# Kernel optimization log

Measured on AMD Instinct MI355X. Metric: run time of the kernel, lower is better.

## Reference

```python
import jax, jax.numpy as jnp
import numpy as np

USER_COUNT = 100000
ITEM_COUNT = 50000
N_NODES = USER_COUNT + ITEM_COUNT
NNZ = 4800000
EMB = 64
BATCH = 4096


def setup_inputs() -> dict:
    key = jax.random.key(0)
    k1, k2, k3, k4, k5, k6, k7 = jax.random.split(key, 7)
    return {
        "user_emb": jax.random.normal(k1, (USER_COUNT, EMB), dtype=jnp.float32),
        "item_emb": jax.random.normal(k2, (ITEM_COUNT, EMB), dtype=jnp.float32),
        "adj_vals": jax.random.uniform(k3, (NNZ,), dtype=jnp.float32),
        "adj_row": jax.random.randint(k4, (NNZ,), 0, N_NODES, dtype=jnp.int64),
        "adj_col": jax.random.randint(k5, (NNZ,), 0, N_NODES, dtype=jnp.int64),
        "users": jax.random.randint(k6, (BATCH,), 0, USER_COUNT, dtype=jnp.int64),
        "items": jax.random.randint(k7, (BATCH,), 0, ITEM_COUNT, dtype=jnp.int64),
        "n_layers": 3,
    }


def _spmm(adj_row, adj_col, adj_vals, x):
    # sparse (N,N) @ dense (N,D): gather source rows, scale by edge values, scatter-add to dest
    msgs = adj_vals[:, None] * x[adj_col]  # [nnz, D]
    return jax.ops.segment_sum(msgs, adj_row, num_segments=N_NODES)


def reference(user_emb, item_emb, adj_vals, adj_row, adj_col, users, items, n_layers):
    ego = jnp.concatenate([user_emb, item_emb], axis=0)  # [N, D]
    for _ in range(n_layers):
        ego = _spmm(adj_row, adj_col, adj_vals, ego)
    user_all = ego[:USER_COUNT]
    item_all = ego[USER_COUNT:]
    return (user_all[users], item_all[items])
```

## Files before the change

### kernel.cpp

```cpp
#include <hip/hip_runtime.h>
#include <hip/hip_bf16.h>

#define USER_COUNT 100000
#define ITEM_COUNT 50000
#define N_NODES    150000
#define EMB        64
#define BATCH      4096

#define NFINE      586
#define FSHIFT     8
#define STRIDE     8960
#define TILE_E     6400

__device__ inline unsigned short f2bf_raw(float f) {
    __hip_bfloat16 h = __float2bfloat16(f);
    unsigned short u; __builtin_memcpy(&u, &h, 2); return u;
}

__global__ __launch_bounds__(256) void zero_kernel(int* __restrict__ p, int n) {
    int i = blockIdx.x * blockDim.x + threadIdx.x;
    if (i < n) p[i] = 0;
}

__global__ __launch_bounds__(512) void partition_kernel(
        const float* __restrict__ vals,
        const int* __restrict__ rows,
        const int* __restrict__ cols,
        int* __restrict__ gcur,
        uint2* __restrict__ fine, int nnz) {
    __shared__ uint2 buf[TILE_E];
    __shared__ unsigned short bid[TILE_E];
    __shared__ int   cnt[NFINE];
    __shared__ int   sloff[NFINE + 1];
    __shared__ int   gb[NFINE];
    __shared__ int   sscan[512];
    const int b = blockIdx.x, t = threadIdx.x;
    const int sbeg = b * TILE_E, send = min(sbeg + TILE_E, nnz);
    const int n = send - sbeg;

    for (int f = t; f < NFINE; f += 512) cnt[f] = 0;
    __syncthreads();
    for (int i = sbeg + t; i < send; i += 512)
        atomicAdd(&cnt[rows[i] >> FSHIFT], 1);
    __syncthreads();
    int c0 = (2 * t < NFINE) ? cnt[2 * t] : 0;
    int c1 = (2 * t + 1 < NFINE) ? cnt[2 * t + 1] : 0;
    sscan[t] = c0 + c1;
    __syncthreads();
    for (int o = 1; o < 512; o <<= 1) {
        int v = (t >= o) ? sscan[t - o] : 0;
        __syncthreads();
        sscan[t] += v;
        __syncthreads();
    }
    int base = (t == 0) ? 0 : sscan[t - 1];
    if (2 * t < NFINE) sloff[2 * t] = base;
    if (2 * t + 1 < NFINE) sloff[2 * t + 1] = base + c0;
    if (t == 511) sloff[NFINE] = sscan[511];
    __syncthreads();
    for (int f = t; f < NFINE; f += 512) {
        int c = cnt[f];
        gb[f] = f * STRIDE + ((c > 0) ? atomicAdd(&gcur[f], c) : 0);
        cnt[f] = sloff[f];
    }
    __syncthreads();
    for (int i = sbeg + t; i < send; i += 512) {
        int r = rows[i];
        int f = r >> FSHIFT;
        int pos = atomicAdd(&cnt[f], 1);
        buf[pos] = make_uint2(__float_as_uint(vals[i]),
                              (unsigned)cols[i] | ((unsigned)(r & 255) << 18));
        bid[pos] = (unsigned short)f;
    }
    __syncthreads();
    for (int idx = t; idx < n; idx += 512) {
        int f = bid[idx];
        fine[gb[f] + (idx - sloff[f])] = buf[idx];
    }
}

__global__ __launch_bounds__(512) void bucket_sort_kernel(
        const uint2* __restrict__ fine,
        const int* __restrict__ tot,
        float2* __restrict__ perm,
        uint2* __restrict__ rp) {
    __shared__ uint2 sbuf[STRIDE];
    __shared__ int hist[256];
    __shared__ int cur[256];
    __shared__ int ss[256];
    const int f   = blockIdx.x;
    const int t   = threadIdx.x;
    const int n   = min(tot[f], STRIDE);
    const int base = f * STRIDE;

    if (t < 256) hist[t] = 0;
    __syncthreads();
    for (int k = t; k < n; k += 512)
        atomicAdd(&hist[(fine[base + k].y >> 18) & 255], 1);
    __syncthreads();
    int v = (t < 256) ? hist[t] : 0;
    if (t < 256) ss[t] = v;
    __syncthreads();
    for (int o = 1; o < 256; o <<= 1) {
        int x = (t < 256 && t >= o) ? ss[t - o] : 0;
        __syncthreads();
        if (t < 256) ss[t] += x;
        __syncthreads();
    }
    if (t < 256) {
        int e = ss[t] - v;
        cur[t] = e;
        int row = (f << FSHIFT) + t;
        if (row < N_NODES)
            rp[row] = make_uint2((unsigned)(base + e),
                                 (unsigned)(base + e + v));
    }
    __syncthreads();
    for (int k = t; k < n; k += 512) {
        uint2 e = fine[base + k];
        int lrow = (e.y >> 18) & 255;
        int pos = atomicAdd(&cur[lrow], 1);
        sbuf[pos] = e;
    }
    __syncthreads();
    for (int k = t; k < n; k += 512) {
        uint2 e = sbuf[k];
        perm[base + k] = make_float2(__uint_as_float(e.x),
                                     __int_as_float((int)(e.y & 0x3FFFFu)));
    }
}

__global__ void to_bf16(const float4* __restrict__ ue,
                        const float4* __restrict__ ie,
                        uint2* __restrict__ xh) {
    int i = blockIdx.x * blockDim.x + threadIdx.x;
    const int n4 = (N_NODES * EMB) / 4;
    const int u4 = (USER_COUNT * EMB) / 4;
    if (i >= n4) return;
    float4 fv = (i < u4) ? ue[i] : ie[i - u4];
    uint2 o;
    o.x = (unsigned int)f2bf_raw(fv.x) | ((unsigned int)f2bf_raw(fv.y) << 16);
    o.y = (unsigned int)f2bf_raw(fv.z) | ((unsigned int)f2bf_raw(fv.w) << 16);
    xh[i] = o;
}

#define ACC8(U, W)                                      \
    a0 += (W) * __uint_as_float((U).x << 16);           \
    a1 += (W) * __uint_as_float((U).x & 0xffff0000u);   \
    a2 += (W) * __uint_as_float((U).y << 16);           \
    a3 += (W) * __uint_as_float((U).y & 0xffff0000u);   \
    a4 += (W) * __uint_as_float((U).z << 16);           \
    a5 += (W) * __uint_as_float((U).z & 0xffff0000u);   \
    a6 += (W) * __uint_as_float((U).w << 16);           \
    a7 += (W) * __uint_as_float((U).w & 0xffff0000u);

__global__ void spmm_bf16(const uint2* __restrict__ rp,
                          const float2* __restrict__ perm,
                          const unsigned short* __restrict__ xh,
                          unsigned short* __restrict__ yh) {
    int wid  = (blockIdx.x * blockDim.x + threadIdx.x) >> 6;
    int lane = threadIdx.x & 63;
    int g    = lane >> 3;
    int s    = lane & 7;
    int r    = (wid << 3) + g;
    if (r >= N_NODES) return;

    uint2 be = rp[r];
    int beg = (int)be.x, end = (int)be.y;

    const uint4* xv = (const uint4*)xh;
    float a0 = 0.f, a1 = 0.f, a2 = 0.f, a3 = 0.f;
    float a4 = 0.f, a5 = 0.f, a6 = 0.f, a7 = 0.f;

    int j = beg;
    for (; j + 7 < end; j += 8) {
        float2 e0 = perm[j];
        float2 e1 = perm[j + 1];
        float2 e2 = perm[j + 2];
        float2 e3 = perm[j + 3];
        float2 e4 = perm[j + 4];
        float2 e5 = perm[j + 5];
        float2 e6 = perm[j + 6];
        float2 e7 = perm[j + 7];
        uint4 u0 = xv[(((long long)__float_as_int(e0.y)) << 3) + s];
        uint4 u1 = xv[(((long long)__float_as_int(e1.y)) << 3) + s];
        uint4 u2 = xv[(((long long)__float_as_int(e2.y)) << 3) + s];
        uint4 u3 = xv[(((long long)__float_as_int(e3.y)) << 3) + s];
        uint4 u4 = xv[(((long long)__float_as_int(e4.y)) << 3) + s];
        uint4 u5 = xv[(((long long)__float_as_int(e5.y)) << 3) + s];
        uint4 u6 = xv[(((long long)__float_as_int(e6.y)) << 3) + s];
        uint4 u7 = xv[(((long long)__float_as_int(e7.y)) << 3) + s];
        ACC8(u0, e0.x) ACC8(u1, e1.x) ACC8(u2, e2.x) ACC8(u3, e3.x)
        ACC8(u4, e4.x) ACC8(u5, e5.x) ACC8(u6, e6.x) ACC8(u7, e7.x)
    }
    for (; j < end; ++j) {
        float2 e = perm[j];
        uint4 u = xv[(((long long)__float_as_int(e.y)) << 3) + s];
        ACC8(u, e.x)
    }

    uint4 o;
    o.x = (unsigned)f2bf_raw(a0) | ((unsigned)f2bf_raw(a1) << 16);
    o.y = (unsigned)f2bf_raw(a2) | ((unsigned)f2bf_raw(a3) << 16);
    o.z = (unsigned)f2bf_raw(a4) | ((unsigned)f2bf_raw(a5) << 16);
    o.w = (unsigned)f2bf_raw(a6) | ((unsigned)f2bf_raw(a7) << 16);
    ((uint4*)yh)[(((long long)r) << 3) + s] = o;
}

__global__ void spmm_batch_kernel(const uint2* __restrict__ rp,
                                  const float2* __restrict__ perm,
                                  const unsigned short* __restrict__ xh,
                                  const int* __restrict__ users,
                                  const int* __restrict__ items,
                                  float4* __restrict__ out) {
    int wid  = (blockIdx.x * blockDim.x + threadIdx.x) >> 6;
    int lane = threadIdx.x & 63;
    int g    = lane >> 3;
    int s    = lane & 7;
    int b    = (wid << 3) + g;
    if (b >= 2 * BATCH) return;
    int node = (b < BATCH) ? users[b] : (USER_COUNT + items[b - BATCH]);

    uint2 be = rp[node];
    int beg = (int)be.x, end = (int)be.y;

    const uint4* xv = (const uint4*)xh;
    float a0 = 0.f, a1 = 0.f, a2 = 0.f, a3 = 0.f;
    float a4 = 0.f, a5 = 0.f, a6 = 0.f, a7 = 0.f;

    int j = beg;
    for (; j + 3 < end; j += 4) {
        float2 e0 = perm[j];
        float2 e1 = perm[j + 1];
        float2 e2 = perm[j + 2];
        float2 e3 = perm[j + 3];
        uint4 u0 = xv[(((long long)__float_as_int(e0.y)) << 3) + s];
        uint4 u1 = xv[(((long long)__float_as_int(e1.y)) << 3) + s];
        uint4 u2 = xv[(((long long)__float_as_int(e2.y)) << 3) + s];
        uint4 u3 = xv[(((long long)__float_as_int(e3.y)) << 3) + s];
        ACC8(u0, e0.x) ACC8(u1, e1.x) ACC8(u2, e2.x) ACC8(u3, e3.x)
    }
    for (; j < end; ++j) {
        float2 e = perm[j];
        uint4 u = xv[(((long long)__float_as_int(e.y)) << 3) + s];
        ACC8(u, e.x)
    }

    out[(size_t)b * 16 + 2 * s]     = make_float4(a0, a1, a2, a3);
    out[(size_t)b * 16 + 2 * s + 1] = make_float4(a4, a5, a6, a7);
}

extern "C" void kernel_launch(void* const* d_in, const int* in_sizes, int n_in,
                              void* d_out, int out_size, void* d_ws, size_t ws_size,
                              hipStream_t stream) {
    const float* user_emb = (const float*)d_in[0];
    const float* item_emb = (const float*)d_in[1];
    const float* adj_vals = (const float*)d_in[2];
    const int*   adj_row  = (const int*)d_in[3];
    const int*   adj_col  = (const int*)d_in[4];
    const int*   users    = (const int*)d_in[5];
    const int*   items    = (const int*)d_in[6];

    const int nnz  = in_sizes[2];
    const int nblk = (nnz + TILE_E - 1) / TILE_E;

    const size_t region = (size_t)NFINE * STRIDE + 1024;

    char* p = (char*)d_ws;
    uint2* fine = (uint2*)p;
    unsigned short* xh_a = (unsigned short*)p;
    unsigned short* xh_b = xh_a + (size_t)N_NODES * EMB;
    p += region * sizeof(uint2);
    float2* perm = (float2*)p;
    p += region * sizeof(float2);
    uint2* rp = (uint2*)p;
    p += (size_t)(N_NODES + 16) * sizeof(uint2);
    int* gcur = (int*)p;
    p += 1024 * sizeof(int);

    zero_kernel<<<4, 256, 0, stream>>>(gcur, 1024);
    partition_kernel<<<nblk, 512, 0, stream>>>(adj_vals, adj_row, adj_col,
                                               gcur, fine, nnz);
    bucket_sort_kernel<<<NFINE, 512, 0, stream>>>(fine, gcur, perm, rp);

    const int n4 = (N_NODES * EMB) / 4;
    to_bf16<<<(n4 + 255) / 256, 256, 0, stream>>>((const float4*)user_emb,
                                                  (const float4*)item_emb,
                                                  (uint2*)xh_a);

    const int spmm_blocks = (N_NODES / 8 + 3) / 4;
    spmm_bf16<<<spmm_blocks, 256, 0, stream>>>(rp, perm, xh_a, xh_b);
    spmm_bf16<<<spmm_blocks, 256, 0, stream>>>(rp, perm, xh_b, xh_a);
    spmm_batch_kernel<<<(2 * BATCH / 8) / 4, 256, 0, stream>>>(
        rp, perm, xh_a, users, items, (float4*)d_out);
}
```

Measured before the change: 406.9 us.

## Fuse bucket sort with first SpMM layer using sorted edges in LDS

```diff
diff --git a/kernel.cpp b/kernel.cpp
--- a/kernel.cpp
+++ b/kernel.cpp
@@ -79,6 +79,16 @@
     }
 }
 
+#define ACC8(U, W)                                      \
+    a0 += (W) * __uint_as_float((U).x << 16);           \
+    a1 += (W) * __uint_as_float((U).x & 0xffff0000u);   \
+    a2 += (W) * __uint_as_float((U).y << 16);           \
+    a3 += (W) * __uint_as_float((U).y & 0xffff0000u);   \
+    a4 += (W) * __uint_as_float((U).z << 16);           \
+    a5 += (W) * __uint_as_float((U).z & 0xffff0000u);   \
+    a6 += (W) * __uint_as_float((U).w << 16);           \
+    a7 += (W) * __uint_as_float((U).w & 0xffff0000u);
+
 __global__ __launch_bounds__(512) void bucket_sort_kernel(
         const uint2* __restrict__ fine,
         const int* __restrict__ tot,
@@ -130,6 +140,102 @@
     }
 }
 
+__global__ __launch_bounds__(512) void sort_spmm_kernel(
+        const uint2* __restrict__ fine,
+        const int* __restrict__ tot,
+        float2* __restrict__ perm,
+        uint2* __restrict__ rp,
+        const unsigned short* __restrict__ xh,
+        unsigned short* __restrict__ yh) {
+    __shared__ uint2 sbuf[STRIDE];
+    __shared__ int hist[256];
+    __shared__ int cur[256];
+    __shared__ int ss[256];
+    __shared__ int rstart[256];
+    const int f   = blockIdx.x;
+    const int t   = threadIdx.x;
+    const int n   = min(tot[f], STRIDE);
+    const int base = f * STRIDE;
+
+    if (t < 256) hist[t] = 0;
+    __syncthreads();
+    for (int k = t; k < n; k += 512)
+        atomicAdd(&hist[(fine[base + k].y >> 18) & 255], 1);
+    __syncthreads();
+    int v = (t < 256) ? hist[t] : 0;
+    if (t < 256) ss[t] = v;
+    __syncthreads();
+    for (int o = 1; o < 256; o <<= 1) {
+        int x = (t < 256 && t >= o) ? ss[t - o] : 0;
+        __syncthreads();
+        if (t < 256) ss[t] += x;
+        __syncthreads();
+    }
+    if (t < 256) {
+        int e = ss[t] - v;
+        rstart[t] = e;
+        cur[t] = e;
+        int row = (f << FSHIFT) + t;
+        if (row < N_NODES)
+            rp[row] = make_uint2((unsigned)(base + e),
+                                 (unsigned)(base + e + v));
+    }
+    __syncthreads();
+    for (int k = t; k < n; k += 512) {
+        uint2 e = fine[base + k];
+        int lrow = (e.y >> 18) & 255;
+        int pos = atomicAdd(&cur[lrow], 1);
+        sbuf[pos] = e;
+    }
+    __syncthreads();
+    for (int k = t; k < n; k += 512) {
+        uint2 e = sbuf[k];
+        perm[base + k] = make_float2(__uint_as_float(e.x),
+                                     __int_as_float((int)(e.y & 0x3FFFFu)));
+    }
+    const int w    = t >> 6;
+    const int lane = t & 63;
+    const int g    = lane >> 3;
+    const int s    = lane & 7;
+    const uint4* xv = (const uint4*)xh;
+    for (int k = 0; k < 4; ++k) {
+        int l = (w << 5) + (k << 3) + g;
+        int r = (f << FSHIFT) + l;
+        if (r >= N_NODES) continue;
+        int j   = rstart[l];
+        int end = cur[l];
+        float a0 = 0.f, a1 = 0.f, a2 = 0.f, a3 = 0.f;
+        float a4 = 0.f, a5 = 0.f, a6 = 0.f, a7 = 0.f;
+        for (; j + 3 < end; j += 4) {
+            uint2 e0 = sbuf[j];
+            uint2 e1 = sbuf[j + 1];
+            uint2 e2 = sbuf[j + 2];
+            uint2 e3 = sbuf[j + 3];
+            uint4 u0 = xv[(((long long)(e0.y & 0x3FFFFu)) << 3) + s];
+            uint4 u1 = xv[(((long long)(e1.y & 0x3FFFFu)) << 3) + s];
+            uint4 u2 = xv[(((long long)(e2.y & 0x3FFFFu)) << 3) + s];
+            uint4 u3 = xv[(((long long)(e3.y & 0x3FFFFu)) << 3) + s];
+            float w0 = __uint_as_float(e0.x);
+            float w1 = __uint_as_float(e1.x);
+            float w2 = __uint_as_float(e2.x);
+            float w3 = __uint_as_float(e3.x);
+            ACC8(u0, w0) ACC8(u1, w1) ACC8(u2, w2) ACC8(u3, w3)
+        }
+        for (; j < end; ++j) {
+            uint2 e = sbuf[j];
+            uint4 u = xv[(((long long)(e.y & 0x3FFFFu)) << 3) + s];
+            float w0 = __uint_as_float(e.x);
+            ACC8(u, w0)
+        }
+        uint4 o;
+        o.x = (unsigned)f2bf_raw(a0) | ((unsigned)f2bf_raw(a1) << 16);
+        o.y = (unsigned)f2bf_raw(a2) | ((unsigned)f2bf_raw(a3) << 16);
+        o.z = (unsigned)f2bf_raw(a4) | ((unsigned)f2bf_raw(a5) << 16);
+        o.w = (unsigned)f2bf_raw(a6) | ((unsigned)f2bf_raw(a7) << 16);
+        ((uint4*)yh)[(((long long)r) << 3) + s] = o;
+    }
+}
+
 __global__ void to_bf16(const float4* __restrict__ ue,
                         const float4* __restrict__ ie,
                         uint2* __restrict__ xh) {
@@ -143,16 +249,6 @@
     o.y = (unsigned int)f2bf_raw(fv.z) | ((unsigned int)f2bf_raw(fv.w) << 16);
     xh[i] = o;
 }
-
-#define ACC8(U, W)                                      \
-    a0 += (W) * __uint_as_float((U).x << 16);           \
-    a1 += (W) * __uint_as_float((U).x & 0xffff0000u);   \
-    a2 += (W) * __uint_as_float((U).y << 16);           \
-    a3 += (W) * __uint_as_float((U).y & 0xffff0000u);   \
-    a4 += (W) * __uint_as_float((U).z << 16);           \
-    a5 += (W) * __uint_as_float((U).z & 0xffff0000u);   \
-    a6 += (W) * __uint_as_float((U).w << 16);           \
-    a7 += (W) * __uint_as_float((U).w & 0xffff0000u);
 
 __global__ void spmm_bf16(const uint2* __restrict__ rp,
                           const float2* __restrict__ perm,
@@ -265,32 +361,53 @@
     const int nblk = (nnz + TILE_E - 1) / TILE_E;
 
     const size_t region = (size_t)NFINE * STRIDE + 1024;
-
-    char* p = (char*)d_ws;
-    uint2* fine = (uint2*)p;
-    unsigned short* xh_a = (unsigned short*)p;
-    unsigned short* xh_b = xh_a + (size_t)N_NODES * EMB;
-    p += region * sizeof(uint2);
-    float2* perm = (float2*)p;
-    p += region * sizeof(float2);
-    uint2* rp = (uint2*)p;
-    p += (size_t)(N_NODES + 16) * sizeof(uint2);
-    int* gcur = (int*)p;
-    p += 1024 * sizeof(int);
-
-    zero_kernel<<<4, 256, 0, stream>>>(gcur, 1024);
-    partition_kernel<<<nblk, 512, 0, stream>>>(adj_vals, adj_row, adj_col,
-                                               gcur, fine, nnz);
-    bucket_sort_kernel<<<NFINE, 512, 0, stream>>>(fine, gcur, perm, rp);
-
+    const size_t xh_sz  = (size_t)N_NODES * EMB * sizeof(unsigned short);
     const int n4 = (N_NODES * EMB) / 4;
-    to_bf16<<<(n4 + 255) / 256, 256, 0, stream>>>((const float4*)user_emb,
-                                                  (const float4*)item_emb,
-                                                  (uint2*)xh_a);
-
     const int spmm_blocks = (N_NODES / 8 + 3) / 4;
-    spmm_bf16<<<spmm_blocks, 256, 0, stream>>>(rp, perm, xh_a, xh_b);
-    spmm_bf16<<<spmm_blocks, 256, 0, stream>>>(rp, perm, xh_b, xh_a);
-    spmm_batch_kernel<<<(2 * BATCH / 8) / 4, 256, 0, stream>>>(
-        rp, perm, xh_a, users, items, (float4*)d_out);
-}
+
+    const size_t need_fused = region * 8 + region * 8 + 2 * xh_sz
+                            + (size_t)(N_NODES + 16) * 8 + 4096;
+
+    if (ws_size >= need_fused) {
+        char* p = (char*)d_ws;
+        uint2* fine = (uint2*)p;            p += region * sizeof(uint2);
+        float2* perm = (float2*)p;          p += region * sizeof(float2);
+        unsigned short* xh_a = (unsigned short*)p;  p += xh_sz;
+        unsigned short* xh_b = (unsigned short*)p;  p += xh_sz;
+        uint2* rp = (uint2*)p;              p += (size_t)(N_NODES + 16) * sizeof(uint2);
+        int* gcur = (int*)p;
+
+        zero_kernel<<<4, 256, 0, stream>>>(gcur, 1024);
+        to_bf16<<<(n4 + 255) / 256, 256, 0, stream>>>(
+            (const float4*)user_emb, (const float4*)item_emb, (uint2*)xh_a);
+        partition_kernel<<<nblk, 512, 0, stream>>>(adj_vals, adj_row, adj_col,
+                                                   gcur, fine, nnz);
+        sort_spmm_kernel<<<NFINE, 512, 0, stream>>>(fine, gcur, perm, rp,
+                                                    xh_a, xh_b);
+        spmm_bf16<<<spmm_blocks, 256, 0, stream>>>(rp, perm, xh_b, xh_a);
+        spmm_batch_kernel<<<(2 * BATCH / 8) / 4, 256, 0, stream>>>(
+            rp, perm, xh_a, users, items, (float4*)d_out);
+    } else {
+        char* p = (char*)d_ws;
+        uint2* fine = (uint2*)p;
+        unsigned short* xh_a = (unsigned short*)p;
+        unsigned short* xh_b = xh_a + (size_t)N_NODES * EMB;
+        p += region * sizeof(uint2);
+        float2* perm = (float2*)p;
+        p += region * sizeof(float2);
+        uint2* rp = (uint2*)p;
+        p += (size_t)(N_NODES + 16) * sizeof(uint2);
+        int* gcur = (int*)p;
+
+        zero_kernel<<<4, 256, 0, stream>>>(gcur, 1024);
+        partition_kernel<<<nblk, 512, 0, stream>>>(adj_vals, adj_row, adj_col,
+                                                   gcur, fine, nnz);
+        bucket_sort_kernel<<<NFINE, 512, 0, stream>>>(fine, gcur, perm, rp);
+        to_bf16<<<(n4 + 255) / 256, 256, 0, stream>>>(
+            (const float4*)user_emb, (const float4*)item_emb, (uint2*)xh_a);
+        spmm_bf16<<<spmm_blocks, 256, 0, stream>>>(rp, perm, xh_a, xh_b);
+        spmm_bf16<<<spmm_blocks, 256, 0, stream>>>(rp, perm, xh_b, xh_a);
+        spmm_batch_kernel<<<(2 * BATCH / 8) / 4, 256, 0, stream>>>(
+            rp, perm, xh_a, users, items, (float4*)d_out);
+    }
+}
```

Measured after the change: 404.6 us. Within noise of the previous version (-0.6%).
